# Performance work log

Measured on AMD Instinct MI355X. Metric: run time of the kernel, lower is better.

Reference implementation:

```python
import jax, jax.numpy as jnp
import numpy as np

B, C_IN, C_OUT, N, E = 4, 16, 16, 16384, 131072
EDGE_CH = 2 * (C_IN + 2)  # 36


def setup_inputs() -> dict:
    key = jax.random.key(0)
    ks = jax.random.split(key, 7)
    u = jax.random.normal(ks[0], (B, C_IN, N), dtype=jnp.float32)
    grid = jax.random.uniform(ks[1], (B, N, 2), dtype=jnp.float32)
    edge_index = jax.random.randint(ks[2], (2, E), 0, N, dtype=jnp.int32)
    k_w1 = jax.random.normal(ks[3], (EDGE_CH, 8), dtype=jnp.float32) / np.sqrt(EDGE_CH)
    k_b1 = jnp.zeros((8,), dtype=jnp.float32)
    k_w2 = jax.random.normal(ks[4], (8, C_IN * C_OUT), dtype=jnp.float32) / np.sqrt(8.0)
    k_b2 = jnp.zeros((C_IN * C_OUT,), dtype=jnp.float32)
    root_w = jax.random.normal(ks[5], (C_IN, C_OUT), dtype=jnp.float32) / np.sqrt(C_IN)
    return {"u": u, "grid": grid, "edge_index": edge_index,
            "k_w1": k_w1, "k_b1": k_b1, "k_w2": k_w2, "k_b2": k_b2,
            "root_w": root_w}


def reference(u, grid, edge_index, k_w1, k_b1, k_w2, k_b2, root_w):
    b, c_in, n = u.shape
    c_out = root_w.shape[1]
    # [B, C, N] -> [B*N, C]
    x = jnp.transpose(u, (0, 2, 1)).reshape(b * n, c_in)
    pf = jnp.concatenate([x, grid.reshape(-1, 2)], axis=-1)  # [B*N, C+2]
    # faithful to edge_index_one.repeat(1,1,B).view(2,-1): tile, NO batch offset
    ei = jnp.tile(edge_index, (1, b))  # [2, E*B]
    src, dst = ei[0], ei[1]
    attr = jnp.concatenate([pf[src], pf[dst]], axis=-1)  # [EB, 2*(C+2)]
    h = jax.nn.gelu(attr @ k_w1 + k_b1, approximate=False)
    w = (h @ k_w2 + k_b2).reshape(-1, c_in, c_out)  # [EB, C_in, C_out]
    msg = jnp.einsum('ec,eco->eo', x[src], w)  # per-edge matmul
    # scatter-mean onto targets (PyG aggr='mean'; empty -> 0)
    num_seg = b * n
    agg = jax.ops.segment_sum(msg, dst, num_segments=num_seg)
    cnt = jax.ops.segment_sum(jnp.ones((msg.shape[0],), msg.dtype), dst,
                              num_segments=num_seg)
    agg = agg / jnp.maximum(cnt, 1.0)[:, None]
    out = agg + x @ root_w  # root_weight=True, bias=False
    return jnp.transpose(out.reshape(b, n, c_out), (0, 2, 1))
```

## Files before the change

kernel.cpp:

```cpp
#include <hip/hip_runtime.h>
#include <math.h>

#define NN 16384
#define NE 131072
#define S2 32

typedef unsigned int uint32;
typedef unsigned short ushort;

__device__ __forceinline__ ushort f2bf(float f) {
    uint32 b = __float_as_uint(f);
    b += 0x7FFFu + ((b >> 16) & 1u);
    return (ushort)(b >> 16);
}
__device__ __forceinline__ float lo16(uint32 u) { return __uint_as_float(u << 16); }
__device__ __forceinline__ float hi16(uint32 u) { return __uint_as_float(u & 0xFFFF0000u); }


__global__ __launch_bounds__(256) void d1_pre(
        const float* __restrict__ u, const float* __restrict__ grid,
        const float* __restrict__ kw1, const float* __restrict__ kb1,
        const float* __restrict__ kw2, const float* __restrict__ kb2,
        const float* __restrict__ root_w,
        ushort* __restrict__ SRC, ushort* __restrict__ HB,
        int* __restrict__ cursor, float* __restrict__ out) {
    int bid = blockIdx.x;
    int t = threadIdx.x;

    if (bid < 256) {
        __shared__ float s_pf[64 * 18];
        __shared__ float s_w1[288];
        __shared__ float s_b1[8];
        __shared__ float s_w2t[16 * 132];
        __shared__ float s_b2t[256];
        int n0 = bid * 64;

        if (t < 64) cursor[n0 + t] = 0;

        for (int i = t; i < 1024; i += 256) {
            int c = i >> 6, nl = i & 63;
            s_pf[nl * 18 + c] = u[c * NN + n0 + nl];
        }
        if (t < 128) {
            int nl = t >> 1, g = t & 1;
            s_pf[nl * 18 + 16 + g] = grid[2 * (n0 + nl) + g];
        }
        if (t < 8) s_b1[t] = kb1[t];
        {
            s_w1[t] = kw1[t];
            if (t < 32) s_w1[256 + t] = kw1[256 + t];
        }
        for (int i = t; i < 2048; i += 256) {
            int j = i >> 8, rem = i & 255, ci = rem >> 4, co = rem & 15;
            s_w2t[co * 132 + j * 16 + ci] = kw2[i];
        }
        {
            int ci = t >> 4, co = t & 15;
            s_b2t[co * 16 + ci] = kb2[ci * 16 + co];
        }
        __syncthreads();

        int co = t & 15;
        #pragma unroll
        for (int s = 0; s < 4; ++s) {
            int nl = s * 16 + (t >> 4);
            int n = n0 + nl;
            ushort* row = SRC + (size_t)n * 160;
            const float* pfl = s_pf + nl * 18;
            float x[16];
            #pragma unroll
            for (int ci = 0; ci < 16; ++ci) x[ci] = pfl[ci];

            {
                float bt = 0.0f;
                const float4* bv = (const float4*)(s_b2t + co * 16);
                #pragma unroll
                for (int q = 0; q < 4; ++q) {
                    float4 w = bv[q];
                    bt += x[4*q] * w.x + x[4*q+1] * w.y + x[4*q+2] * w.z + x[4*q+3] * w.w;
                }
                row[8 + co] = f2bf(bt);
            }
            {
                ushort gp[8];
                #pragma unroll
                for (int j = 0; j < 8; ++j) {
                    float g = 0.0f;
                    const float4* wv = (const float4*)(s_w2t + co * 132 + j * 16);
                    #pragma unroll
                    for (int q = 0; q < 4; ++q) {
                        float4 w = wv[q];
                        g += x[4*q] * w.x + x[4*q+1] * w.y + x[4*q+2] * w.z + x[4*q+3] * w.w;
                    }
                    gp[j] = f2bf(g);
                }
                uint4 pk;
                pk.x = (uint32)gp[0] | ((uint32)gp[1] << 16);
                pk.y = (uint32)gp[2] | ((uint32)gp[3] << 16);
                pk.z = (uint32)gp[4] | ((uint32)gp[5] << 16);
                pk.w = (uint32)gp[6] | ((uint32)gp[7] << 16);
                *(uint4*)(row + 24 + co * 8) = pk;
            }
            if (co < 8) {
                float hv = s_b1[co];
                #pragma unroll
                for (int i = 0; i < 18; ++i) hv += pfl[i] * s_w1[i * 8 + co];
                row[co] = f2bf(hv);
            } else {
                int jj = co - 8;
                float hv = 0.0f;
                #pragma unroll
                for (int i = 0; i < 18; ++i) hv += pfl[i] * s_w1[(18 + i) * 8 + jj];
                HB[n * 8 + jj] = f2bf(hv);
            }
        }
    } else {
        __shared__ float s_rw[256];
        s_rw[t] = root_w[t];
        __syncthreads();
        int idx = (bid - 256) * 256 + t;
        int b = (idx >> 14) + 1;
        int n = idx & (NN - 1);
        float xx[16];
        #pragma unroll
        for (int c = 0; c < 16; ++c) xx[c] = u[(b * 16 + c) * NN + n];
        float acc[16];
        #pragma unroll
        for (int co = 0; co < 16; ++co) acc[co] = 0.0f;
        #pragma unroll
        for (int c = 0; c < 16; ++c) {
            float xv = xx[c];
            #pragma unroll
            for (int co = 0; co < 16; ++co) acc[co] += xv * s_rw[c * 16 + co];
        }
        #pragma unroll
        for (int co = 0; co < 16; ++co) out[(b * 16 + co) * NN + n] = acc[co];
    }
}

__global__ __launch_bounds__(256) void d2_edge(
        const int* __restrict__ ei,
        const ushort* __restrict__ SRC, const ushort* __restrict__ HB,
        int* __restrict__ cursor, float* __restrict__ ebuf) {
    int e = blockIdx.x * 256 + threadIdx.x;
    int s = ei[e];
    int d = ei[NE + e];

    const ushort* row = SRC + (size_t)s * 160;
    uint4 ht = *(const uint4*)(row);
    uint4 hb = *(const uint4*)(HB + d * 8);

    float pre[8] = {
        lo16(ht.x) + lo16(hb.x), hi16(ht.x) + hi16(hb.x),
        lo16(ht.y) + lo16(hb.y), hi16(ht.y) + hi16(hb.y),
        lo16(ht.z) + lo16(hb.z), hi16(ht.z) + hi16(hb.z),
        lo16(ht.w) + lo16(hb.w), hi16(ht.w) + hi16(hb.w)
    };
    float h[8];
    #pragma unroll
    for (int j = 0; j < 8; ++j)
        h[j] = 0.5f * pre[j] * (1.0f + erff(pre[j] * 0.70710678118654752f));

    float msg[16];
    {
        uint4 bt0 = *(const uint4*)(row + 8);
        uint4 bt1 = *(const uint4*)(row + 16);
        msg[0]  = lo16(bt0.x); msg[1]  = hi16(bt0.x);
        msg[2]  = lo16(bt0.y); msg[3]  = hi16(bt0.y);
        msg[4]  = lo16(bt0.z); msg[5]  = hi16(bt0.z);
        msg[6]  = lo16(bt0.w); msg[7]  = hi16(bt0.w);
        msg[8]  = lo16(bt1.x); msg[9]  = hi16(bt1.x);
        msg[10] = lo16(bt1.y); msg[11] = hi16(bt1.y);
        msg[12] = lo16(bt1.z); msg[13] = hi16(bt1.z);
        msg[14] = lo16(bt1.w); msg[15] = hi16(bt1.w);
    }
    #pragma unroll
    for (int co = 0; co < 16; ++co) {
        uint4 g = *(const uint4*)(row + 24 + co * 8);
        float acc = msg[co];
        acc += h[0] * lo16(g.x);
        acc += h[1] * hi16(g.x);
        acc += h[2] * lo16(g.y);
        acc += h[3] * hi16(g.y);
        acc += h[4] * lo16(g.z);
        acc += h[5] * hi16(g.z);
        acc += h[6] * lo16(g.w);
        acc += h[7] * hi16(g.w);
        msg[co] = acc;
    }

    int pos = atomicAdd(&cursor[d], 1);
    if (pos < S2) {
        float4* o = (float4*)(ebuf + ((size_t)d * S2 + pos) * 16);
        o[0] = make_float4(msg[0],  msg[1],  msg[2],  msg[3]);
        o[1] = make_float4(msg[4],  msg[5],  msg[6],  msg[7]);
        o[2] = make_float4(msg[8],  msg[9],  msg[10], msg[11]);
        o[3] = make_float4(msg[12], msg[13], msg[14], msg[15]);
    }
}

__global__ __launch_bounds__(256) void d3_out(
        const int* __restrict__ cursor, const float* __restrict__ ebuf,
        const float* __restrict__ u, const float* __restrict__ root_w,
        float* __restrict__ out) {
    __shared__ float s_rw[256];
    __shared__ float s_o[256];
    int t = threadIdx.x;
    s_rw[t] = root_w[t];
    __syncthreads();
    int n0 = blockIdx.x * 16;
    int nl = t >> 4, co = t & 15;
    int n = n0 + nl;
    int cnt = cursor[n];
    int deg = min(cnt, S2);
    const float* base = ebuf + (size_t)n * S2 * 16 + co;
    float sum = 0.0f;
    for (int k = 0; k < deg; ++k) sum += base[k * 16];
    float acc = sum / fmaxf((float)cnt, 1.0f);
    #pragma unroll
    for (int c = 0; c < 16; ++c) acc += u[c * NN + n] * s_rw[c * 16 + co];
    s_o[co * 16 + nl] = acc;
    __syncthreads();
    int co2 = t >> 4, nl2 = t & 15;
    out[co2 * NN + n0 + nl2] = s_o[co2 * 16 + nl2];
}

extern "C" void kernel_launch(void* const* d_in, const int* in_sizes, int n_in,
                              void* d_out, int out_size, void* d_ws, size_t ws_size,
                              hipStream_t stream) {
    const float* u      = (const float*)d_in[0];
    const float* grid   = (const float*)d_in[1];
    const int*   ei     = (const int*)  d_in[2];
    const float* kw1    = (const float*)d_in[3];
    const float* kb1    = (const float*)d_in[4];
    const float* kw2    = (const float*)d_in[5];
    const float* kb2    = (const float*)d_in[6];
    const float* root_w = (const float*)d_in[7];
    float* out = (float*)d_out;

    ushort* SRC    = (ushort*)d_ws;
    ushort* HB     = SRC + (size_t)NN * 160;
    float*  ebuf   = (float*)(HB + (size_t)NN * 8);
    int*    cursor = (int*)(ebuf + (size_t)NN * S2 * 16);

    d1_pre<<<256 + 192, 256, 0, stream>>>(u, grid, kw1, kb1, kw2, kb2, root_w,
                                          SRC, HB, cursor, out);
    d2_edge<<<NE / 256, 256, 0, stream>>>(ei, SRC, HB, cursor, ebuf);
    d3_out<<<NN / 16, 256, 0, stream>>>(cursor, ebuf, u, root_w, out);
}
```

Measured before the change: 39.30 us.

## Bucket edges by source node so the edge kernel reuses source rows

```diff
diff --git a/kernel.cpp b/kernel.cpp
--- a/kernel.cpp
+++ b/kernel.cpp
@@ -4,6 +4,7 @@
 #define NN 16384
 #define NE 131072
 #define S2 32
+#define SPB 32
 
 typedef unsigned int uint32;
 typedef unsigned short ushort;
@@ -17,13 +18,19 @@
 __device__ __forceinline__ float hi16(uint32 u) { return __uint_as_float(u & 0xFFFF0000u); }
 
 
-__global__ __launch_bounds__(256) void d1_pre(
+__global__ __launch_bounds__(256) void k0_zero(int4* __restrict__ p) {
+    p[blockIdx.x * 256 + threadIdx.x] = make_int4(0, 0, 0, 0);
+}
+
+__global__ __launch_bounds__(256) void k1_pre(
         const float* __restrict__ u, const float* __restrict__ grid,
+        const int* __restrict__ ei,
         const float* __restrict__ kw1, const float* __restrict__ kb1,
         const float* __restrict__ kw2, const float* __restrict__ kb2,
         const float* __restrict__ root_w,
         ushort* __restrict__ SRC, ushort* __restrict__ HB,
-        int* __restrict__ cursor, float* __restrict__ out) {
+        int* __restrict__ scur, int* __restrict__ sdst,
+        float* __restrict__ out) {
     int bid = blockIdx.x;
     int t = threadIdx.x;
 
@@ -34,8 +41,6 @@
         __shared__ float s_w2t[16 * 132];
         __shared__ float s_b2t[256];
         int n0 = bid * 64;
-
-        if (t < 64) cursor[n0 + t] = 0;
 
         for (int i = t; i < 1024; i += 256) {
             int c = i >> 6, nl = i & 63;
@@ -114,7 +119,7 @@
                 HB[n * 8 + jj] = f2bf(hv);
             }
         }
-    } else {
+    } else if (bid < 448) {
         __shared__ float s_rw[256];
         s_rw[t] = root_w[t];
         __syncthreads();
@@ -135,71 +140,102 @@
         }
         #pragma unroll
         for (int co = 0; co < 16; ++co) out[(b * 16 + co) * NN + n] = acc[co];
+    } else {
+        int e = (bid - 448) * 256 + t;
+        int s = ei[e];
+        int d = ei[NE + e];
+        int pos = atomicAdd(&scur[s], 1);
+        if (pos < S2) sdst[s * S2 + pos] = d;
     }
 }
 
-__global__ __launch_bounds__(256) void d2_edge(
-        const int* __restrict__ ei,
+__global__ __launch_bounds__(256) void k2_edge(
         const ushort* __restrict__ SRC, const ushort* __restrict__ HB,
+        const int* __restrict__ scur, const int* __restrict__ sdst,
         int* __restrict__ cursor, float* __restrict__ ebuf) {
-    int e = blockIdx.x * 256 + threadIdx.x;
-    int s = ei[e];
-    int d = ei[NE + e];
-
-    const ushort* row = SRC + (size_t)s * 160;
-    uint4 ht = *(const uint4*)(row);
-    uint4 hb = *(const uint4*)(HB + d * 8);
-
-    float pre[8] = {
-        lo16(ht.x) + lo16(hb.x), hi16(ht.x) + hi16(hb.x),
-        lo16(ht.y) + lo16(hb.y), hi16(ht.y) + hi16(hb.y),
-        lo16(ht.z) + lo16(hb.z), hi16(ht.z) + hi16(hb.z),
-        lo16(ht.w) + lo16(hb.w), hi16(ht.w) + hi16(hb.w)
-    };
-    float h[8];
-    #pragma unroll
-    for (int j = 0; j < 8; ++j)
-        h[j] = 0.5f * pre[j] * (1.0f + erff(pre[j] * 0.70710678118654752f));
-
-    float msg[16];
-    {
-        uint4 bt0 = *(const uint4*)(row + 8);
-        uint4 bt1 = *(const uint4*)(row + 16);
-        msg[0]  = lo16(bt0.x); msg[1]  = hi16(bt0.x);
-        msg[2]  = lo16(bt0.y); msg[3]  = hi16(bt0.y);
-        msg[4]  = lo16(bt0.z); msg[5]  = hi16(bt0.z);
-        msg[6]  = lo16(bt0.w); msg[7]  = hi16(bt0.w);
-        msg[8]  = lo16(bt1.x); msg[9]  = hi16(bt1.x);
-        msg[10] = lo16(bt1.y); msg[11] = hi16(bt1.y);
-        msg[12] = lo16(bt1.z); msg[13] = hi16(bt1.z);
-        msg[14] = lo16(bt1.w); msg[15] = hi16(bt1.w);
+    __shared__ int s_pref[SPB + 1];
+    int t = threadIdx.x;
+    int n0 = blockIdx.x * SPB;
+
+    if (t < SPB) {
+        int dg = min(scur[n0 + t], S2);
+        int v = dg;
+        #pragma unroll
+        for (int off = 1; off < SPB; off <<= 1) {
+            int w = __shfl_up(v, off);
+            if (t >= off) v += w;
+        }
+        s_pref[t + 1] = v;
+        if (t == 0) s_pref[0] = 0;
     }
-    #pragma unroll
-    for (int co = 0; co < 16; ++co) {
-        uint4 g = *(const uint4*)(row + 24 + co * 8);
-        float acc = msg[co];
-        acc += h[0] * lo16(g.x);
-        acc += h[1] * hi16(g.x);
-        acc += h[2] * lo16(g.y);
-        acc += h[3] * hi16(g.y);
-        acc += h[4] * lo16(g.z);
-        acc += h[5] * hi16(g.z);
-        acc += h[6] * lo16(g.w);
-        acc += h[7] * hi16(g.w);
-        msg[co] = acc;
+    __syncthreads();
+    int total = s_pref[SPB];
+
+    for (int i = t; i < total; i += 256) {
+        int lo = 0, hi = SPB;
+        while (hi - lo > 1) {
+            int mid = (lo + hi) >> 1;
+            if (s_pref[mid] <= i) lo = mid; else hi = mid;
+        }
+        int s = n0 + lo;
+        int slot = i - s_pref[lo];
+        int d = sdst[s * S2 + slot];
+
+        const ushort* row = SRC + (size_t)s * 160;
+        uint4 ht = *(const uint4*)(row);
+        uint4 hb = *(const uint4*)(HB + d * 8);
+
+        float pre[8] = {
+            lo16(ht.x) + lo16(hb.x), hi16(ht.x) + hi16(hb.x),
+            lo16(ht.y) + lo16(hb.y), hi16(ht.y) + hi16(hb.y),
+            lo16(ht.z) + lo16(hb.z), hi16(ht.z) + hi16(hb.z),
+            lo16(ht.w) + lo16(hb.w), hi16(ht.w) + hi16(hb.w)
+        };
+        float h[8];
+        #pragma unroll
+        for (int j = 0; j < 8; ++j)
+            h[j] = 0.5f * pre[j] * (1.0f + erff(pre[j] * 0.70710678118654752f));
+
+        float msg[16];
+        {
+            uint4 bt0 = *(const uint4*)(row + 8);
+            uint4 bt1 = *(const uint4*)(row + 16);
+            msg[0]  = lo16(bt0.x); msg[1]  = hi16(bt0.x);
+            msg[2]  = lo16(bt0.y); msg[3]  = hi16(bt0.y);
+            msg[4]  = lo16(bt0.z); msg[5]  = hi16(bt0.z);
+            msg[6]  = lo16(bt0.w); msg[7]  = hi16(bt0.w);
+            msg[8]  = lo16(bt1.x); msg[9]  = hi16(bt1.x);
+            msg[10] = lo16(bt1.y); msg[11] = hi16(bt1.y);
+            msg[12] = lo16(bt1.z); msg[13] = hi16(bt1.z);
+            msg[14] = lo16(bt1.w); msg[15] = hi16(bt1.w);
+        }
+        #pragma unroll
+        for (int co = 0; co < 16; ++co) {
+            uint4 g = *(const uint4*)(row + 24 + co * 8);
+            float acc = msg[co];
+            acc += h[0] * lo16(g.x);
+            acc += h[1] * hi16(g.x);
+            acc += h[2] * lo16(g.y);
+            acc += h[3] * hi16(g.y);
+            acc += h[4] * lo16(g.z);
+            acc += h[5] * hi16(g.z);
+            acc += h[6] * lo16(g.w);
+            acc += h[7] * hi16(g.w);
+            msg[co] = acc;
+        }
+
+        int pos = atomicAdd(&cursor[d], 1);
+        if (pos < S2) {
+            float4* o = (float4*)(ebuf + ((size_t)d * S2 + pos) * 16);
+            o[0] = make_float4(msg[0],  msg[1],  msg[2],  msg[3]);
+            o[1] = make_float4(msg[4],  msg[5],  msg[6],  msg[7]);
+            o[2] = make_float4(msg[8],  msg[9],  msg[10], msg[11]);
+            o[3] = make_float4(msg[12], msg[13], msg[14], msg[15]);
+        }
     }
-
-    int pos = atomicAdd(&cursor[d], 1);
-    if (pos < S2) {
-        float4* o = (float4*)(ebuf + ((size_t)d * S2 + pos) * 16);
-        o[0] = make_float4(msg[0],  msg[1],  msg[2],  msg[3]);
-        o[1] = make_float4(msg[4],  msg[5],  msg[6],  msg[7]);
-        o[2] = make_float4(msg[8],  msg[9],  msg[10], msg[11]);
-        o[3] = make_float4(msg[12], msg[13], msg[14], msg[15]);
-    }
-}
-
-__global__ __launch_bounds__(256) void d3_out(
+}
+
+__global__ __launch_bounds__(256) void k3_out(
         const int* __restrict__ cursor, const float* __restrict__ ebuf,
         const float* __restrict__ u, const float* __restrict__ root_w,
         float* __restrict__ out) {
@@ -242,9 +278,12 @@
     ushort* HB     = SRC + (size_t)NN * 160;
     float*  ebuf   = (float*)(HB + (size_t)NN * 8);
     int*    cursor = (int*)(ebuf + (size_t)NN * S2 * 16);
-
-    d1_pre<<<256 + 192, 256, 0, stream>>>(u, grid, kw1, kb1, kw2, kb2, root_w,
-                                          SRC, HB, cursor, out);
-    d2_edge<<<NE / 256, 256, 0, stream>>>(ei, SRC, HB, cursor, ebuf);
-    d3_out<<<NN / 16, 256, 0, stream>>>(cursor, ebuf, u, root_w, out);
-}
+    int*    scur   = cursor + NN;
+    int*    sdst   = scur + NN;
+
+    k0_zero<<<32, 256, 0, stream>>>((int4*)cursor);
+    k1_pre<<<960, 256, 0, stream>>>(u, grid, ei, kw1, kb1, kw2, kb2, root_w,
+                                    SRC, HB, scur, sdst, out);
+    k2_edge<<<NN / SPB, 256, 0, stream>>>(SRC, HB, scur, sdst, cursor, ebuf);
+    k3_out<<<NN / 16, 256, 0, stream>>>(cursor, ebuf, u, root_w, out);
+}
```

After: 47.42 us. +20.6%, slower.
